# Kernel optimization log

Measured on AMD Instinct MI355X. Metric: run time of the kernel, lower is better.

Reference implementation:

```python
import jax, jax.numpy as jnp
import numpy as np

B, C, L, M, EMB, HID = 32, 64, 8192, 32, 256, 64

def setup_inputs() -> dict:
    key = jax.random.key(0)
    ks = jax.random.split(key, 14)
    s_w = 1.0 / (C * C)
    s_a = 1.0 / EMB
    return {
        "x": jax.random.normal(ks[0], (B, C, L), jnp.float32),
        "emb": jax.random.normal(ks[1], (B, EMB), jnp.float32),
        "weights_pos": s_w * jax.random.normal(ks[2], (C, C, M, 2), jnp.float32),
        "weights_neg": s_w * jax.random.normal(ks[3], (C, C, M, 2), jnp.float32),
        "A_real_pos": s_a * jax.random.normal(ks[4], (M, EMB), jnp.float32),
        "A_imag_pos": s_a * jax.random.normal(ks[5], (M, EMB), jnp.float32),
        "A_real_neg": s_a * jax.random.normal(ks[6], (M, EMB), jnp.float32),
        "A_imag_neg": s_a * jax.random.normal(ks[7], (M, EMB), jnp.float32),
        "tm_w1": 0.05 * jax.random.normal(ks[8], (HID, EMB), jnp.float32),
        "tm_b1": jnp.zeros((HID,), jnp.float32),
        "tm_w2": 0.05 * jax.random.normal(ks[9], (2 * C, HID), jnp.float32),
        "tm_b2": jnp.zeros((2 * C,), jnp.float32),
        "lin_w": 0.05 * jax.random.normal(ks[10], (C, C), jnp.float32),
        "lin_b": jnp.zeros((C,), jnp.float32),
    }

def reference(x, emb, weights_pos, weights_neg, A_real_pos, A_imag_pos,
              A_real_neg, A_imag_neg, tm_w1, tm_b1, tm_w2, tm_b2, lin_w, lin_b):
    b, c, l = x.shape
    m = weights_pos.shape[2]
    k = l // 2 + 1
    # ---- SpectralConv1d branch ----
    x_ft = jnp.fft.rfft(x, norm="ortho")  # [B,C,K] complex
    wp = weights_pos[..., 0] + 1j * weights_pos[..., 1]  # [Ci,Co,M]
    wn = weights_neg[..., 0] + 1j * weights_neg[..., 1]
    phi_p = (emb @ A_real_pos.T) + 1j * (emb @ A_imag_pos.T)  # [B,M]
    phi_n = (emb @ A_real_neg.T) + 1j * (emb @ A_imag_neg.T)
    out_pos = jnp.einsum("bim,iom->bom", x_ft[:, :, :m], wp) * phi_p[:, None, :]
    out_neg = jnp.einsum("bim,iom->bom", x_ft[:, :, k - m:], wn) * phi_n[:, None, :]
    out_ft = jnp.zeros((b, c, k), dtype=x_ft.dtype)
    out_ft = out_ft.at[:, :, :m].set(out_pos).at[:, :, k - m:].set(out_neg)
    x1 = jnp.fft.irfft(out_ft, n=l, norm="ortho")  # [B,C,L]
    # ---- Conv1DTime branch (FiLM-style) ----
    h = jax.nn.silu(emb @ tm_w1.T + tm_b1)          # [B,HID]
    gb = h @ tm_w2.T + tm_b2                         # [B,2C]
    gamma, beta = gb[:, :c], gb[:, c:]
    xl = jnp.einsum("bcl,oc->bol", x, lin_w) + lin_b[None, :, None]
    x2 = xl * (1.0 + gamma[:, :, None]) + beta[:, :, None]
    return jax.nn.silu(x1 + x2)
```

## Files before the change

### kernel.cpp

```cpp
#include <hip/hip_runtime.h>
#include <math.h>

#define L_ 8192
#define EMB_ 256
#define HID_ 64

typedef __attribute__((ext_vector_type(8))) short bf16x8;
typedef __attribute__((ext_vector_type(4))) float f32x4;
typedef __attribute__((ext_vector_type(4))) int i32x4;

#define OFF_TFB  0
#define OFF_TLB  262144
#define OFF_AFB  524288
#define OFF_XFRP 917504
#define OFF_B2   3014656
#define OFF_PHI  3016704
#define OFF_GB   3020800
#define OFF_WT   3024896
#define OFF_XT   3549184

__device__ inline int pkbf(float a, float b) {
    int r;
    asm volatile("v_cvt_pk_bf16_f32 %0, %1, %2" : "=v"(r) : "v"(a), "v"(b));
    return r;
}
__device__ inline bf16x8 asbf(i32x4 v) { union { i32x4 i; bf16x8 h; } u; u.i = v; return u.h; }
#define MFMA(A,B,C) __builtin_amdgcn_mfma_f32_16x16x32_bf16((A),(B),(C),0,0,0)

__device__ inline ushort f2bf(float v) {
    unsigned b = __float_as_uint(v);
    return (ushort)((b + 0x7FFFu + ((b >> 16) & 1u)) >> 16);
}
__device__ inline float bf2f(ushort h) { return __uint_as_float(((unsigned)h) << 16); }
__device__ inline float hwsin(float rev) { float r; asm("v_sin_f32 %0, %1" : "=v"(r) : "v"(rev)); return r; }
__device__ inline float hwcos(float rev) { float r; asm("v_cos_f32 %0, %1" : "=v"(r) : "v"(rev)); return r; }
__device__ inline unsigned permb(unsigned hi, unsigned lo, unsigned sel) {
    unsigned r;
    asm("v_perm_b32 %0, %1, %2, %3" : "=v"(r) : "v"(hi), "v"(lo), "v"(sel));
    return r;
}

__global__ __launch_bounds__(256) void k_init(ushort* __restrict__ TLB, ushort* __restrict__ TFB,
        const float* __restrict__ emb,
        const float* __restrict__ Arp, const float* __restrict__ Aip,
        const float* __restrict__ Arn, const float* __restrict__ Ain, float* __restrict__ phi,
        const float* __restrict__ w1, const float* __restrict__ b1,
        const float* __restrict__ w2, const float* __restrict__ b2, float* __restrict__ gb,
        const float* __restrict__ wpos, const float* __restrict__ wneg, float* __restrict__ WT) {
    int bid = blockIdx.x;
    if (bid < 4096) {
        int idx = bid * 256 + threadIdx.x;
        int f, l; ushort* dst;
        if (idx < 524288) {
            int u = idx;
            int e = u & 7, lane = (u >> 3) & 63, ct = (u >> 9) & 3, kstep = u >> 11;
            l = kstep * 32 + ((lane >> 4) << 3) + e;
            f = ct * 16 + (lane & 15);
            dst = TLB + u;
        } else {
            int u = idx - 524288;
            int e = u & 7, lane = (u >> 3) & 63, ts = (u >> 9) & 1, lt = u >> 10;
            l = lt * 16 + (lane & 15);
            f = ts * 32 + ((lane >> 4) << 3) + e;
            dst = TFB + u;
        }
        int fr = f & 31; bool sinp = (f & 32) != 0;
        int r = (fr * l) & (L_ - 1);
        float rev = (float)r * (1.0f / (float)L_);
        float v = sinp ? hwsin(rev) : hwcos(rev);
        *dst = f2bf(v);
    } else if (bid < 4112) {
        int tid = (bid - 4096) * 256 + threadIdx.x;
        int b = tid >> 7;
        int mm = (tid >> 2) & 31;
        int cmp = tid & 3;
        const float* A = (cmp == 0) ? Arp : (cmp == 1) ? Aip : (cmp == 2) ? Arn : Ain;
        const float4* e4 = (const float4*)(emb + b * EMB_);
        const float4* a4 = (const float4*)(A + mm * EMB_);
        float acc = 0.f;
        for (int q = 0; q < EMB_ / 4; ++q) {
            float4 ev = e4[q], av = a4[q];
            acc += ev.x * av.x + ev.y * av.y + ev.z * av.z + ev.w * av.w;
        }
        phi[tid] = acc;
    } else if (bid < 4144) {
        __shared__ float h[HID_];
        int b = bid - 4112, t = threadIdx.x;
        if (t < HID_) {
            const float4* e4 = (const float4*)(emb + b * EMB_);
            const float4* w4 = (const float4*)(w1 + t * EMB_);
            float acc = b1[t];
            for (int q = 0; q < EMB_ / 4; ++q) {
                float4 ev = e4[q], wv = w4[q];
                acc += ev.x * wv.x + ev.y * wv.y + ev.z * wv.z + ev.w * wv.w;
            }
            h[t] = acc / (1.f + expf(-acc));
        }
        __syncthreads();
        if (t < 128) {
            float g = b2[t];
            const float4* h4 = (const float4*)h;
            const float4* w4 = (const float4*)(w2 + t * HID_);
            for (int q = 0; q < HID_ / 4; ++q) {
                float4 hv = h4[q], wv = w4[q];
                g += hv.x * wv.x + hv.y * wv.y + hv.z * wv.z + hv.w * wv.w;
            }
            if (t < 64) gb[(b * 64 + t) * 2 + 0] = 1.f + g;
            else        gb[(b * 64 + (t - 64)) * 2 + 1] = g;
        }
    } else {
        int t = bid - 4144;
        int side = t >> 6, i = t & 63;
        const float* W = side ? wneg : wpos;
        const float* src = W + (size_t)i * 4096;
        int tid = threadIdx.x;
        #pragma unroll
        for (int j = 0; j < 8; ++j) {
            int u = tid + 256 * j;
            int mm = u >> 6, o = u & 63;
            float2 v = *(const float2*)(src + o * 64 + mm * 2);
            *(float2*)(WT + ((size_t)(side * 32 + mm)) * 8192 + i * 128 + o * 2) = v;
        }
    }
}

__global__ __launch_bounds__(256, 4) void k_dft(const float* __restrict__ x,
        const ushort* __restrict__ TLB, float* __restrict__ xfrp, unsigned* __restrict__ XT2) {
    __shared__ float sP[4][16][132];
    int stripe = blockIdx.x >> 3;
    int lseg = blockIdx.x & 7;
    int w = threadIdx.x >> 6;
    int lane = threadIdx.x & 63;
    int row = lane & 15, koff = (lane >> 4) << 3;
    int r0 = stripe * 16;
    int kb0 = lseg * 1024 + w * 256;

    f32x4 acc[8];
    #pragma unroll
    for (int i = 0; i < 8; ++i) acc[i] = (f32x4){0.f, 0.f, 0.f, 0.f};

    const float* ap = x + (size_t)(r0 + row) * L_ + kb0 + koff;
    const i32x4* tb = (const i32x4*)TLB;
    int tbase = (kb0 >> 5) * 256 + lane;
    const i32x4 SM = {(int)0x80000000, (int)0x80000000, (int)0x80000000, (int)0x80000000};
    unsigned* xtb = XT2 + ((size_t)stripe * 4096 + ((kb0 + koff) >> 1)) * 16 + row;

    i32x4 hs[8];
    float4 xa0 = *(const float4*)(ap);
    float4 xc0 = *(const float4*)(ap + 4);
    float4 xa1 = *(const float4*)(ap + 32);
    float4 xc1 = *(const float4*)(ap + 36);
    #pragma unroll
    for (int ks = 0; ks < 8; ++ks) {
        float4 nxa = {0,0,0,0}, nxc = {0,0,0,0};
        if (ks < 6) {
            nxa = *(const float4*)(ap + (ks + 2) * 32);
            nxc = *(const float4*)(ap + (ks + 2) * 32 + 4);
        }
        int ti = tbase + ks * 256;
        i32x4 t0 = tb[ti], t1 = tb[ti + 64], t2 = tb[ti + 128], t3 = tb[ti + 192];
        int h0 = pkbf(xa0.x, xa0.y), h1 = pkbf(xa0.z, xa0.w);
        int h2 = pkbf(xc0.x, xc0.y), h3 = pkbf(xc0.z, xc0.w);
        hs[ks] = (i32x4){h0, h1, h2, h3};
        bf16x8 AH = asbf(hs[ks]);
        acc[0] = MFMA(AH, asbf(t0), acc[0]); acc[4] = MFMA(AH, asbf(t0 ^ SM), acc[4]);
        acc[1] = MFMA(AH, asbf(t1), acc[1]); acc[5] = MFMA(AH, asbf(t1 ^ SM), acc[5]);
        acc[2] = MFMA(AH, asbf(t2), acc[2]); acc[6] = MFMA(AH, asbf(t2 ^ SM), acc[6]);
        acc[3] = MFMA(AH, asbf(t3), acc[3]); acc[7] = MFMA(AH, asbf(t3 ^ SM), acc[7]);
        xa0 = xa1; xc0 = xc1; xa1 = nxa; xc1 = nxc;
    }
    #pragma unroll
    for (int ks = 0; ks < 8; ++ks) {
        unsigned* xtp = xtb + (size_t)(ks * 16) * 16;
        xtp[0]  = (unsigned)hs[ks][0];
        xtp[16] = (unsigned)hs[ks][1];
        xtp[32] = (unsigned)hs[ks][2];
        xtp[48] = (unsigned)hs[ks][3];
    }
    int crow = (lane >> 4) << 2;
    int ccol = lane & 15;
    #pragma unroll
    for (int ct = 0; ct < 8; ++ct)
        #pragma unroll
        for (int r = 0; r < 4; ++r)
            sP[w][crow + r][ct * 16 + ccol] = acc[ct][r];
    __syncthreads();
    #pragma unroll
    for (int i = 0; i < 8; ++i) {
        int e = threadIdx.x + 256 * i;
        int rr = e & 15, cc = e >> 4;
        float s = sP[0][rr][cc] + sP[1][rr][cc] + sP[2][rr][cc] + sP[3][rr][cc];
        xfrp[((size_t)(lseg * 128 + cc)) * 2048 + r0 + rr] = s;
    }
}

__global__ __launch_bounds__(256) void k_mix(const float* __restrict__ xfrt,
        const float* __restrict__ WT,
        const float* __restrict__ phi, const float* __restrict__ lw,
        const float* __restrict__ lb, const float* __restrict__ gb,
        ushort* __restrict__ afb, float* __restrict__ bias2) {
    int bi = blockIdx.x;
    int tid = threadIdx.x;
    if (bi >= 256) {
        int b = bi - 256;
        ushort* dst = afb + (size_t)b * 24576;
        #pragma unroll
        for (int j = 0; j < 16; ++j) {
            int u = tid + 256 * j;
            int e = u & 7, lane = (u >> 3) & 63, mt = (u >> 9) & 3, ks2 = u >> 11;
            int c = mt * 16 + (lane & 15);
            int kk = ((lane >> 4) << 3) + e;
            float v = lw[c * 64 + ks2 * 32 + kk] * gb[(b * 64 + c) * 2];
            ushort hi = f2bf(v);
            int base = (((4 + ks2) * 4 + mt) * 64 + lane) * 16;
            dst[base + e] = hi;
            dst[base + 8 + e] = f2bf(v - bf2f(hi));
        }
        if (tid < 64) {
            float g1 = gb[(b * 64 + tid) * 2], be = gb[(b * 64 + tid) * 2 + 1];
            bias2[b * 64 + tid] = lb[tid] * g1 + be;
        }
        return;
    }
    __shared__ float sW[64][64][2];
    __shared__ float sXr[8][64], sXi[8][64];
    int bh = bi & 3, side = (bi >> 2) & 1, mm = bi >> 3;
    int slot = side ? (31 - mm) : mm;
    int colR = side ? (64 + slot) : mm;
    int colI = side ? (96 + slot) : (32 + mm);

    {
        const float4* wt = (const float4*)(WT + ((size_t)(side * 32 + mm)) * 8192);
        float* sWlin = &sW[0][0][0];
        #pragma unroll
        for (int j = 0; j < 8; ++j) {
            int u = tid + 256 * j;
            *(float4*)&sWlin[u * 4] = wt[u];
        }
    }
    {
        const float2* pR = (const float2*)(xfrt + (size_t)colR * 2048 + bh * 512);
        const float2* pI = (const float2*)(xfrt + (size_t)colI * 2048 + bh * 512);
        float2 aR = {0, 0}, aI = {0, 0};
        #pragma unroll
        for (int s = 0; s < 8; ++s) {
            float2 vR = pR[(size_t)s * 131072 + tid];
            float2 vI = pI[(size_t)s * 131072 + tid];
            aR.x += vR.x; aR.y += vR.y;
            aI.x += vI.x; aI.y += vI.y;
        }
        if (!side) { aI.x = -aI.x; aI.y = -aI.y; }
        *(float2*)&sXr[tid >> 5][(tid & 31) * 2] = aR;
        *(float2*)&sXi[tid >> 5][(tid & 31) * 2] = aI;
    }
    __syncthreads();

    int o = tid & 63, bg = tid >> 6;
    const float invL = 1.f / (float)L_;
    float fac = (slot == 0) ? invL : 2.f * invL;
    int comp = side ? 2 : 0;
    int e = slot & 7, kgrp = slot >> 3;
    int mt = o >> 4, lane = kgrp * 16 + (o & 15);
    #pragma unroll
    for (int bl = 0; bl < 2; ++bl) {
        int b_local = bg * 2 + bl;
        int b = bh * 8 + b_local;
        float sre = 0.f, sim = 0.f;
        #pragma unroll 16
        for (int i = 0; i < 64; ++i) {
            float wr = sW[i][o][0], wi = sW[i][o][1];
            float xr = sXr[b_local][i], xi = sXi[b_local][i];
            sre += xr * wr - xi * wi;
            sim += xr * wi + xi * wr;
        }
        const float* ph = &phi[(b * 32 + mm) * 4 + (side ? 2 : 0)];
        float phr = ph[0], phim = ph[1];
        float Pre = sre * phr - sim * phim;
        float Pim = sre * phim + sim * phr;
        float a = fac * Pre;
        float bcoef = (slot == 0) ? 0.f : (side ? 2.f * invL * Pim : -2.f * invL * Pim);
        ushort* dst = afb + (size_t)b * 24576;
        ushort hiA = f2bf(a);
        int baseA = ((comp * 4 + mt) * 64 + lane) * 16;
        dst[baseA + e] = hiA;
        dst[baseA + 8 + e] = f2bf(a - bf2f(hiA));
        ushort hiB = f2bf(bcoef);
        int baseB = (((comp + 1) * 4 + mt) * 64 + lane) * 16;
        dst[baseB + e] = hiB;
        dst[baseB + 8 + e] = f2bf(bcoef - bf2f(hiB));
    }
}

#define TPART(ts)                                                                        \
    {                                                                                    \
        i32x4 bh_[2];                                                                    \
        _Pragma("unroll")                                                                \
        for (int nj = 0; nj < 2; ++nj)                                                   \
            bh_[nj] = tb[((lt0 + nj) * 2 + (ts)) * 64 + lane];                           \
        _Pragma("unroll")                                                                \
        for (int mt = 0; mt < 4; ++mt) {                                                 \
            i32x4 ah0 = ab[(((ts) * 4 + mt) * 64 + lane) * 2];                           \
            i32x4 ah1 = ab[(((2 + (ts)) * 4 + mt) * 64 + lane) * 2];                     \
            bf16x8 AH0 = asbf(ah0), AH1 = asbf(ah1);                                     \
            _Pragma("unroll")                                                            \
            for (int nj = 0; nj < 2; ++nj) {                                             \
                acc[mt][nj] = MFMA(AH0, asbf(bh_[nj]), acc[mt][nj]);                     \
                acc[mt][nj] = MFMA(AH1, asbf(bh_[nj] ^ SM), acc[mt][nj]);                \
            }                                                                            \
        }                                                                                \
    }

#define XPART(ts, xv0, xv1)                                                              \
    {                                                                                    \
        bf16x8 XH0 = asbf(xv0), XH1 = asbf(xv1);                                         \
        _Pragma("unroll")                                                                \
        for (int mt = 0; mt < 4; ++mt) {                                                 \
            i32x4 ah = ab[(((4 + (ts)) * 4 + mt) * 64 + lane) * 2];                      \
            bf16x8 AH = asbf(ah);                                                        \
            acc[mt][0] = MFMA(AH, XH0, acc[mt][0]);                                      \
            acc[mt][1] = MFMA(AH, XH1, acc[mt][1]);                                      \
        }                                                                                \
    }

#define XEXTRACT(q0, q1, dstvar)                                                         \
    dstvar = (i32x4){                                                                    \
        (int)permb((unsigned)q0[1], (unsigned)q0[0], sel),                               \
        (int)permb((unsigned)q0[3], (unsigned)q0[2], sel),                               \
        (int)permb((unsigned)q1[1], (unsigned)q1[0], sel),                               \
        (int)permb((unsigned)q1[3], (unsigned)q1[2], sel)};

__global__ __launch_bounds__(256, 3) void k_fuse(const unsigned* __restrict__ XT2,
        const ushort* __restrict__ TFB, const ushort* __restrict__ AFB,
        const float* __restrict__ bias2, float* __restrict__ out) {
    int b = blockIdx.x >> 6, lt = blockIdx.x & 63;
    int w = threadIdx.x >> 6, lane = threadIdx.x & 63;
    int col = lane & 15, kgrp = lane >> 4;
    int lbase = lt * 128 + w * 32;
    int lt0 = lbase >> 4;
    const i32x4* tb = (const i32x4*)TFB;
    const i32x4* ab = (const i32x4*)AFB + (size_t)b * 3072;
    const i32x4* xt4 = (const i32x4*)XT2;

    f32x4 acc[4][2];
    #pragma unroll
    for (int i = 0; i < 4; ++i)
        #pragma unroll
        for (int j = 0; j < 2; ++j) acc[i][j] = (f32x4){0.f, 0.f, 0.f, 0.f};

    int sm = (col & 1) ? (int)0x80008000 : 0;
    i32x4 SM = {sm, sm, sm, sm};
    unsigned sel = (col & 1) ? 0x07060302u : 0x05040100u;

    size_t i00 = ((size_t)(b * 4 + (kgrp >> 1)) * 4096 + ((lbase + col) >> 1)) * 4 + (kgrp & 1) * 2;
    size_t i01 = i00 + 8 * 4;
    size_t i10 = i00 + (size_t)2 * 4096 * 4;
    size_t i11 = i10 + 8 * 4;
    i32x4 q000 = xt4[i00], q001 = xt4[i00 + 1];
    i32x4 q010 = xt4[i01], q011 = xt4[i01 + 1];
    i32x4 q100 = xt4[i10], q101 = xt4[i10 + 1];
    i32x4 q110 = xt4[i11], q111 = xt4[i11 + 1];

    TPART(0)
    i32x4 xv00, xv01;
    XEXTRACT(q000, q001, xv00)
    XEXTRACT(q010, q011, xv01)
    XPART(0, xv00, xv01)
    TPART(1)
    i32x4 xv10, xv11;
    XEXTRACT(q100, q101, xv10)
    XEXTRACT(q110, q111, xv11)
    XPART(1, xv10, xv11)

    #pragma unroll
    for (int mt = 0; mt < 4; ++mt) {
        #pragma unroll
        for (int r = 0; r < 4; ++r) {
            int c = mt * 16 + kgrp * 4 + r;
            float bias = bias2[b * 64 + c];
            float* op = out + (size_t)(b * 64 + c) * L_ + lbase + col;
            #pragma unroll
            for (int nj = 0; nj < 2; ++nj) {
                float v = acc[mt][nj][r] + bias;
                op[nj * 16] = v / (1.f + __expf(-v));
            }
        }
    }
}

extern "C" void kernel_launch(void* const* d_in, const int* in_sizes, int n_in,
                              void* d_out, int out_size, void* d_ws, size_t ws_size,
                              hipStream_t stream) {
    const float* x    = (const float*)d_in[0];
    const float* emb  = (const float*)d_in[1];
    const float* wpos = (const float*)d_in[2];
    const float* wneg = (const float*)d_in[3];
    const float* Arp  = (const float*)d_in[4];
    const float* Aip  = (const float*)d_in[5];
    const float* Arn  = (const float*)d_in[6];
    const float* Ain  = (const float*)d_in[7];
    const float* w1   = (const float*)d_in[8];
    const float* b1   = (const float*)d_in[9];
    const float* w2   = (const float*)d_in[10];
    const float* b2   = (const float*)d_in[11];
    const float* lw   = (const float*)d_in[12];
    const float* lb   = (const float*)d_in[13];
    float* out = (float*)d_out;
    float* ws = (float*)d_ws;
    ushort*   TFB  = (ushort*)(ws + OFF_TFB);
    ushort*   TLB  = (ushort*)(ws + OFF_TLB);
    ushort*   AFB  = (ushort*)(ws + OFF_AFB);
    float*    XFRP = ws + OFF_XFRP;
    float*    B2   = ws + OFF_B2;
    float*    PHI  = ws + OFF_PHI;
    float*    GB   = ws + OFF_GB;
    float*    WT   = ws + OFF_WT;
    unsigned* XT2  = (unsigned*)(ws + OFF_XT);

    hipLaunchKernelGGL(k_init,  dim3(4272), dim3(256), 0, stream,
                       TLB, TFB, emb, Arp, Aip, Arn, Ain, PHI, w1, b1, w2, b2, GB,
                       wpos, wneg, WT);
    hipLaunchKernelGGL(k_dft,   dim3(1024), dim3(256), 0, stream, x, TLB, XFRP, XT2);
    hipLaunchKernelGGL(k_mix,   dim3(288),  dim3(256), 0, stream, XFRP, WT, PHI,
                       lw, lb, GB, AFB, B2);
    hipLaunchKernelGGL(k_fuse,  dim3(2048), dim3(256), 0, stream, XT2, TFB, AFB, B2, out);
}
```

Measured before the change: 66.41 us.

## Stage x tiles through LDS for coalesced loads and vectorized XT2 stores

```diff
diff --git a/kernel.cpp b/kernel.cpp
--- a/kernel.cpp
+++ b/kernel.cpp
@@ -126,12 +126,12 @@
 
 __global__ __launch_bounds__(256, 4) void k_dft(const float* __restrict__ x,
         const ushort* __restrict__ TLB, float* __restrict__ xfrp, unsigned* __restrict__ XT2) {
-    __shared__ float sP[4][16][132];
+    __shared__ float sP[2][16][132];
+    __shared__ unsigned sX[4][16][68];
     int stripe = blockIdx.x >> 3;
     int lseg = blockIdx.x & 7;
     int w = threadIdx.x >> 6;
     int lane = threadIdx.x & 63;
-    int row = lane & 15, koff = (lane >> 4) << 3;
     int r0 = stripe * 16;
     int kb0 = lseg * 1024 + w * 256;
 
@@ -139,57 +139,86 @@
     #pragma unroll
     for (int i = 0; i < 8; ++i) acc[i] = (f32x4){0.f, 0.f, 0.f, 0.f};
 
-    const float* ap = x + (size_t)(r0 + row) * L_ + kb0 + koff;
     const i32x4* tb = (const i32x4*)TLB;
     int tbase = (kb0 >> 5) * 256 + lane;
     const i32x4 SM = {(int)0x80000000, (int)0x80000000, (int)0x80000000, (int)0x80000000};
-    unsigned* xtb = XT2 + ((size_t)stripe * 4096 + ((kb0 + koff) >> 1)) * 16 + row;
-
-    i32x4 hs[8];
-    float4 xa0 = *(const float4*)(ap);
-    float4 xc0 = *(const float4*)(ap + 4);
-    float4 xa1 = *(const float4*)(ap + 32);
-    float4 xc1 = *(const float4*)(ap + 36);
-    #pragma unroll
-    for (int ks = 0; ks < 8; ++ks) {
-        float4 nxa = {0,0,0,0}, nxc = {0,0,0,0};
-        if (ks < 6) {
-            nxa = *(const float4*)(ap + (ks + 2) * 32);
-            nxc = *(const float4*)(ap + (ks + 2) * 32 + 4);
-        }
-        int ti = tbase + ks * 256;
-        i32x4 t0 = tb[ti], t1 = tb[ti + 64], t2 = tb[ti + 128], t3 = tb[ti + 192];
-        int h0 = pkbf(xa0.x, xa0.y), h1 = pkbf(xa0.z, xa0.w);
-        int h2 = pkbf(xc0.x, xc0.y), h3 = pkbf(xc0.z, xc0.w);
-        hs[ks] = (i32x4){h0, h1, h2, h3};
-        bf16x8 AH = asbf(hs[ks]);
-        acc[0] = MFMA(AH, asbf(t0), acc[0]); acc[4] = MFMA(AH, asbf(t0 ^ SM), acc[4]);
-        acc[1] = MFMA(AH, asbf(t1), acc[1]); acc[5] = MFMA(AH, asbf(t1 ^ SM), acc[5]);
-        acc[2] = MFMA(AH, asbf(t2), acc[2]); acc[6] = MFMA(AH, asbf(t2 ^ SM), acc[6]);
-        acc[3] = MFMA(AH, asbf(t3), acc[3]); acc[7] = MFMA(AH, asbf(t3 ^ SM), acc[7]);
-        xa0 = xa1; xc0 = xc1; xa1 = nxa; xc1 = nxc;
-    }
-    #pragma unroll
-    for (int ks = 0; ks < 8; ++ks) {
-        unsigned* xtp = xtb + (size_t)(ks * 16) * 16;
-        xtp[0]  = (unsigned)hs[ks][0];
-        xtp[16] = (unsigned)hs[ks][1];
-        xtp[32] = (unsigned)hs[ks][2];
-        xtp[48] = (unsigned)hs[ks][3];
+
+    int lrow2 = lane >> 5;
+    int lcol = (lane & 31) * 4;
+    int jw = (lane & 31) * 2;
+    int frow = lane & 15;
+    int fj = (lane >> 4) * 4;
+
+    #pragma unroll
+    for (int c = 0; c < 2; ++c) {
+        int cbase = kb0 + c * 128;
+        float4 f0 = *(const float4*)(x + (size_t)(r0 + 0  + lrow2) * L_ + cbase + lcol);
+        float4 f1 = *(const float4*)(x + (size_t)(r0 + 2  + lrow2) * L_ + cbase + lcol);
+        float4 f2 = *(const float4*)(x + (size_t)(r0 + 4  + lrow2) * L_ + cbase + lcol);
+        float4 f3 = *(const float4*)(x + (size_t)(r0 + 6  + lrow2) * L_ + cbase + lcol);
+        float4 f4 = *(const float4*)(x + (size_t)(r0 + 8  + lrow2) * L_ + cbase + lcol);
+        float4 f5 = *(const float4*)(x + (size_t)(r0 + 10 + lrow2) * L_ + cbase + lcol);
+        float4 f6 = *(const float4*)(x + (size_t)(r0 + 12 + lrow2) * L_ + cbase + lcol);
+        float4 f7 = *(const float4*)(x + (size_t)(r0 + 14 + lrow2) * L_ + cbase + lcol);
+        #define STG(i, fv)                                                   \
+            {                                                                \
+                unsigned d0 = (unsigned)pkbf(fv.x, fv.y);                    \
+                unsigned d1 = (unsigned)pkbf(fv.z, fv.w);                    \
+                sX[w][i * 2 + lrow2][jw]     = d0;                           \
+                sX[w][i * 2 + lrow2][jw + 1] = d1;                           \
+            }
+        STG(0, f0) STG(1, f1) STG(2, f2) STG(3, f3)
+        STG(4, f4) STG(5, f5) STG(6, f6) STG(7, f7)
+        #undef STG
+        #pragma unroll
+        for (int ks = 0; ks < 4; ++ks) {
+            i32x4 av = *(const i32x4*)&sX[w][frow][ks * 16 + fj];
+            bf16x8 AH = asbf(av);
+            int ti = tbase + (c * 4 + ks) * 256;
+            i32x4 t0 = tb[ti], t1 = tb[ti + 64], t2 = tb[ti + 128], t3 = tb[ti + 192];
+            acc[0] = MFMA(AH, asbf(t0), acc[0]); acc[4] = MFMA(AH, asbf(t0 ^ SM), acc[4]);
+            acc[1] = MFMA(AH, asbf(t1), acc[1]); acc[5] = MFMA(AH, asbf(t1 ^ SM), acc[5]);
+            acc[2] = MFMA(AH, asbf(t2), acc[2]); acc[6] = MFMA(AH, asbf(t2 ^ SM), acc[6]);
+            acc[3] = MFMA(AH, asbf(t3), acc[3]); acc[7] = MFMA(AH, asbf(t3 ^ SM), acc[7]);
+        }
+        {
+            unsigned* xtc = XT2 + ((size_t)stripe * 4096 + (cbase >> 1)) * 16;
+            int ch4 = (lane & 3) * 4;
+            #pragma unroll
+            for (int q = 0; q < 4; ++q) {
+                int j = q * 16 + (lane >> 2);
+                uint4 v;
+                v.x = sX[w][ch4 + 0][j];
+                v.y = sX[w][ch4 + 1][j];
+                v.z = sX[w][ch4 + 2][j];
+                v.w = sX[w][ch4 + 3][j];
+                *(uint4*)(xtc + (size_t)(q * 256 + lane * 4)) = v;
+            }
+        }
     }
     int crow = (lane >> 4) << 2;
     int ccol = lane & 15;
-    #pragma unroll
-    for (int ct = 0; ct < 8; ++ct)
-        #pragma unroll
-        for (int r = 0; r < 4; ++r)
-            sP[w][crow + r][ct * 16 + ccol] = acc[ct][r];
+    if (w < 2) {
+        #pragma unroll
+        for (int ct = 0; ct < 8; ++ct)
+            #pragma unroll
+            for (int r = 0; r < 4; ++r)
+                sP[w][crow + r][ct * 16 + ccol] = acc[ct][r];
+    }
+    __syncthreads();
+    if (w >= 2) {
+        #pragma unroll
+        for (int ct = 0; ct < 8; ++ct)
+            #pragma unroll
+            for (int r = 0; r < 4; ++r)
+                sP[w - 2][crow + r][ct * 16 + ccol] += acc[ct][r];
+    }
     __syncthreads();
     #pragma unroll
     for (int i = 0; i < 8; ++i) {
         int e = threadIdx.x + 256 * i;
         int rr = e & 15, cc = e >> 4;
-        float s = sP[0][rr][cc] + sP[1][rr][cc] + sP[2][rr][cc] + sP[3][rr][cc];
+        float s = sP[0][rr][cc] + sP[1][rr][cc];
         xfrp[((size_t)(lseg * 128 + cc)) * 2048 + r0 + rr] = s;
     }
 }
```

After: 66.18 us (median of 2 runs). About the same (-0.3%).
